# Performance work log

Hardware: AMD Instinct MI355X
Metric: run time of the kernel (lower is better)

## Reference

```python
import jax, jax.numpy as jnp
import numpy as np

BATCH, SEQ, D_MODEL = 8, 4096, 1024
N, K, RHO_MAX, N_POWER_ITER = 16, 4, 0.3, 2
P = N * (N - 1) // 2  # 120 skew params


def _xavier(key, shape, gain):
    fan_out, fan_in = shape
    std = gain * np.sqrt(2.0 / (fan_in + fan_out))
    return jax.random.normal(key, shape, jnp.float32) * std


def setup_inputs() -> dict:
    key = jax.random.key(0)
    k0, k1, k2, k3 = jax.random.split(key, 4)
    u = jax.random.normal(k0, (BATCH, SEQ, D_MODEL), jnp.float32)
    W_proj_w = _xavier(k1, (P, D_MODEL), 0.1)
    W_proj_b = jnp.zeros((P,), jnp.float32)
    B_w = _xavier(k2, (N, D_MODEL), 0.5)
    C_w = _xavier(k3, (D_MODEL, N), 0.5)
    D = jnp.zeros((D_MODEL,), jnp.float32)
    return {"u": u, "W_proj_w": W_proj_w, "W_proj_b": W_proj_b, "B_w": B_w, "C_w": C_w, "D": D}


def _normalize(x, axis):
    # F.normalize: x / max(||x||, eps)
    return x / jnp.maximum(jnp.linalg.norm(x, axis=axis, keepdims=True), 1e-12)


def reference(u, W_proj_w, W_proj_b, B_w, C_w, D):
    Bsz, T, d = u.shape
    n = B_w.shape[0]
    rows, cols = np.triu_indices(n, 1)

    # 1. skew params for all timesteps at once: (B,T,P)
    v = u @ W_proj_w.T + W_proj_b
    A = jnp.zeros((Bsz, T, n, n), u.dtype)
    A = A.at[..., rows, cols].set(v).at[..., cols, rows].set(-v)

    # 2. spectral-norm scaling (power iteration runs with no grad in torch)
    A_sg = jax.lax.stop_gradient(A)
    u_vec = _normalize(jax.random.normal(jax.random.key(1), (Bsz, T, n, 1), u.dtype), axis=2)
    for _ in range(N_POWER_ITER):
        v_vec = _normalize(jnp.swapaxes(A_sg, -1, -2) @ u_vec, axis=2)
        u_vec = _normalize(A_sg @ v_vec, axis=2)
    sigma = jnp.abs((jnp.swapaxes(u_vec, -1, -2) @ (A @ v_vec))[..., 0, 0])  # (B,T)
    scale = RHO_MAX / jnp.maximum(sigma, RHO_MAX)
    A = A * scale[..., None, None]

    # 3. Neumann-Cayley, k=4 radix-2 splitting: W = (I-A)(I+A^2)(I-A)
    I = jnp.eye(n, dtype=u.dtype)
    ImA = I - A
    W = (ImA @ (I + A @ A)) @ ImA  # (B,T,n,n)

    # orthogonality deviation (monitoring, no grad)
    W_sg = jax.lax.stop_gradient(W)
    WtW = jnp.swapaxes(W_sg, -1, -2) @ W_sg
    ortho_dev = jnp.mean(jnp.linalg.norm(WtW - I, axis=(-2, -1)))

    # 4. sequential state recurrence h_t = W_t h_{t-1} + B u_t via scan
    Bx = u @ B_w.T  # (B,T,n)

    def step(h, inp):
        W_t, bx_t = inp  # (B,n,n), (B,n)
        h = jnp.einsum('bij,bj->bi', W_t, h) + bx_t
        return h, h

    h0 = jnp.zeros((Bsz, n), u.dtype)
    _, hs = jax.lax.scan(step, h0, (jnp.swapaxes(W, 0, 1), jnp.swapaxes(Bx, 0, 1)))
    h_all = jnp.swapaxes(hs, 0, 1)  # (B,T,n)

    y = h_all @ C_w.T + u * D
    return y, ortho_dev
```

## Files before the change

kernel.cpp:

```cpp
#include <hip/hip_runtime.h>
#include <hip/hip_bf16.h>
#include <math.h>

#define BATCHN 8
#define SEQN 4096
#define DMODEL 1024
#define MTOT (BATCHN*SEQN)
#define VB_STRIDE 136
#define CHUNKS 64
#define CLEN 64
#define YSIZE ((size_t)MTOT*DMODEL)
#define BN_ROWS 144

typedef __attribute__((ext_vector_type(8))) short short8;
typedef __attribute__((ext_vector_type(4))) float f32x4;

__device__ __forceinline__ unsigned short f2bf(float x){
  __hip_bfloat16 h = __float2bfloat16(x);
  return *(unsigned short*)&h;
}
__device__ __forceinline__ float bf2f(unsigned short b){
  __hip_bfloat16 h; *(unsigned short*)&h = b;
  return __bfloat162float(h);
}

__device__ __forceinline__ unsigned rotl32(unsigned x, int d){ return (x<<d)|(x>>(32-d)); }
__device__ __forceinline__ void tfr(unsigned &x0, unsigned &x1, int r){ x0 += x1; x1 = rotl32(x1,r); x1 ^= x0; }

__device__ __forceinline__ float xla_erfinv(float x){
  float w = -log1pf(-x*x);
  float p;
  if (w < 5.0f){
    w = w - 2.5f;
    p = 2.81022636e-08f;
    p = fmaf(p, w, 3.43273939e-07f);
    p = fmaf(p, w, -3.5233877e-06f);
    p = fmaf(p, w, -4.39150654e-06f);
    p = fmaf(p, w, 0.00021858087f);
    p = fmaf(p, w, -0.00125372503f);
    p = fmaf(p, w, -0.00417768164f);
    p = fmaf(p, w, 0.246640727f);
    p = fmaf(p, w, 1.50140941f);
  } else {
    w = sqrtf(w) - 3.0f;
    p = -0.000200214257f;
    p = fmaf(p, w, 0.000100950558f);
    p = fmaf(p, w, 0.00134934322f);
    p = fmaf(p, w, -0.00367342844f);
    p = fmaf(p, w, 0.00573950773f);
    p = fmaf(p, w, -0.0076224613f);
    p = fmaf(p, w, 0.00943887047f);
    p = fmaf(p, w, 1.00167406f);
    p = fmaf(p, w, 2.83297682f);
  }
  return p * x;
}

__device__ float jax_randn(unsigned I){
  unsigned x0 = 0u, x1 = I;
  const unsigned ks2 = 0x1BD11BDBu;
  x0 += 0u; x1 += 1u;
  tfr(x0,x1,13); tfr(x0,x1,15); tfr(x0,x1,26); tfr(x0,x1,6);
  x0 += 1u; x1 += ks2 + 1u;
  tfr(x0,x1,17); tfr(x0,x1,29); tfr(x0,x1,16); tfr(x0,x1,24);
  x0 += ks2; x1 += 0u + 2u;
  tfr(x0,x1,13); tfr(x0,x1,15); tfr(x0,x1,26); tfr(x0,x1,6);
  x0 += 0u; x1 += 1u + 3u;
  tfr(x0,x1,17); tfr(x0,x1,29); tfr(x0,x1,16); tfr(x0,x1,24);
  x0 += 1u; x1 += ks2 + 4u;
  tfr(x0,x1,13); tfr(x0,x1,15); tfr(x0,x1,26); tfr(x0,x1,6);
  x0 += ks2; x1 += 0u + 5u;
  unsigned bits = x0 ^ x1;
  unsigned fb = (bits >> 9) | 0x3f800000u;
  float f = __uint_as_float(fb) - 1.0f;
  const float lo = -0.99999994f;
  float val = f * 2.0f + lo;
  val = fmaxf(lo, val);
  return 1.4142135381698608f * xla_erfinv(val);
}

__global__ __launch_bounds__(256) void k0_presplit(const float* __restrict__ Wp,
    const float* __restrict__ Bw, unsigned short* __restrict__ Bhi,
    unsigned short* __restrict__ Blo){
  int i = blockIdx.x*256 + threadIdx.x;
  if (i >= BN_ROWS*DMODEL/4) return;
  int n = i >> 8;
  int k = (i & 255) * 4;
  float4 t = make_float4(0.f,0.f,0.f,0.f);
  if (n < 120)      t = *(const float4*)(Wp + (size_t)n*DMODEL + k);
  else if (n < 136) t = *(const float4*)(Bw + (size_t)(n-120)*DMODEL + k);
  unsigned short h[4], l[4];
  float v[4] = {t.x,t.y,t.z,t.w};
  #pragma unroll
  for (int j=0;j<4;j++){
    h[j] = f2bf(v[j]);
    l[j] = f2bf(v[j] - bf2f(h[j]));
  }
  size_t off = (size_t)n*DMODEL + k;
  *(ushort4*)(Bhi + off) = make_ushort4(h[0],h[1],h[2],h[3]);
  *(ushort4*)(Blo + off) = make_ushort4(l[0],l[1],l[2],l[3]);
}

__global__ __launch_bounds__(128) void k1_mfma(const float* __restrict__ u,
    const unsigned short* __restrict__ Bhi, const unsigned short* __restrict__ Blo,
    const float* __restrict__ Wpb, float* __restrict__ vb){
  __shared__ unsigned short As_hi[64*40];
  __shared__ unsigned short As_lo[64*40];
  __shared__ unsigned short Bs_hi[BN_ROWS*40];
  __shared__ unsigned short Bs_lo[BN_ROWS*40];

  const int tid  = threadIdx.x;
  const int wave = tid >> 6;
  const int lane = tid & 63;
  const int quad = lane >> 4;
  const int lrow = lane & 15;
  const int m0   = blockIdx.x * 64;

  float biasv[9];
  #pragma unroll
  for (int t=0;t<9;t++){
    int col = t*16 + lrow;
    biasv[t] = (col < 120) ? Wpb[col] : 0.f;
  }

  f32x4 acc[2][9];
  #pragma unroll
  for (int s=0;s<2;s++)
    #pragma unroll
    for (int t=0;t<9;t++)
      acc[s][t] = (f32x4){0.f,0.f,0.f,0.f};

  const int arow = tid & 63;
  const int ak0  = (tid >> 6) * 16;

  for (int c=0;c<DMODEL/32;c++){
    {
      const float* src = u + (size_t)(m0+arow)*DMODEL + c*32 + ak0;
      float va[16];
      #pragma unroll
      for (int q=0;q<4;q++){
        float4 t4 = *(const float4*)(src + q*4);
        va[q*4+0]=t4.x; va[q*4+1]=t4.y; va[q*4+2]=t4.z; va[q*4+3]=t4.w;
      }
      unsigned short hh[16], ll[16];
      #pragma unroll
      for (int j=0;j<16;j++){
        hh[j] = f2bf(va[j]);
        ll[j] = f2bf(va[j] - bf2f(hh[j]));
      }
      unsigned short* dh = As_hi + arow*40 + ak0;
      unsigned short* dl = As_lo + arow*40 + ak0;
      #pragma unroll
      for (int half=0; half<2; half++){
        short8 ph, pl;
        #pragma unroll
        for (int j=0;j<8;j++){ ph[j] = (short)hh[half*8+j]; pl[j] = (short)ll[half*8+j]; }
        *(short8*)(dh + half*8) = ph;
        *(short8*)(dl + half*8) = pl;
      }
    }
    for (int i = tid; i < BN_ROWS*4; i += 128){
      int n  = i >> 2;
      int kq = (i & 3) * 8;
      size_t goff = (size_t)n*DMODEL + c*32 + kq;
      *(short8*)(Bs_hi + n*40 + kq) = *(const short8*)(Bhi + goff);
      *(short8*)(Bs_lo + n*40 + kq) = *(const short8*)(Blo + goff);
    }
    __syncthreads();

    short8 ahi[2], alo[2];
    #pragma unroll
    for (int s=0;s<2;s++){
      int row = wave*32 + s*16 + lrow;
      ahi[s] = *(const short8*)(As_hi + row*40 + quad*8);
      alo[s] = *(const short8*)(As_lo + row*40 + quad*8);
    }
    #pragma unroll
    for (int t=0;t<9;t++){
      short8 bhi = *(const short8*)(Bs_hi + (t*16+lrow)*40 + quad*8);
      short8 blo = *(const short8*)(Bs_lo + (t*16+lrow)*40 + quad*8);
      #pragma unroll
      for (int s=0;s<2;s++){
        acc[s][t] = __builtin_amdgcn_mfma_f32_16x16x32_bf16(ahi[s], bhi, acc[s][t], 0,0,0);
        acc[s][t] = __builtin_amdgcn_mfma_f32_16x16x32_bf16(ahi[s], blo, acc[s][t], 0,0,0);
        acc[s][t] = __builtin_amdgcn_mfma_f32_16x16x32_bf16(alo[s], bhi, acc[s][t], 0,0,0);
      }
    }
    __syncthreads();
  }

  #pragma unroll
  for (int s=0;s<2;s++){
    #pragma unroll
    for (int t=0;t<9;t++){
      int col = t*16 + lrow;
      if (col < VB_STRIDE){
        #pragma unroll
        for (int i=0;i<4;i++){
          int row = m0 + wave*32 + s*16 + quad*4 + i;
          vb[(size_t)row*VB_STRIDE + col] = acc[s][t][i] + biasv[t];
        }
      }
    }
  }
}

__global__ __launch_bounds__(128) void k2_build_w(const float* __restrict__ vb,
    float* __restrict__ Wg, float* __restrict__ ortho){
  __shared__ float Af[8*324];
  __shared__ float Sf[8*324];
  __shared__ float gsum[8];
  const int tid = threadIdx.x;
  const int grp = tid >> 4;
  const int r   = tid & 15;
  const int m   = blockIdx.x*8 + grp;
  float* A = Af + grp*324;
  float* S = Sf + grp*324;
  const float* vrow = vb + (size_t)m*VB_STRIDE;

  float a_s[16];
  #pragma unroll
  for (int c=0;c<16;c++){
    float val = 0.f;
    if (c > r)      val =  vrow[r*15 - (r*(r-1))/2 + (c-r-1)];
    else if (c < r) val = -vrow[c*15 - (c*(c-1))/2 + (r-c-1)];
    a_s[c] = val;
  }

  float uv = jax_randn((unsigned)m*16u + (unsigned)r);
  float nn = uv*uv;
  #pragma unroll
  for (int s=1;s<16;s<<=1) nn += __shfl_xor(nn, s, 16);
  uv = uv / fmaxf(sqrtf(nn), 1e-12f);

  float t2 = 0.f;
  #pragma unroll
  for (int it=0; it<2; ++it){
    float t1 = 0.f;
    #pragma unroll
    for (int k=0;k<16;k++) t1 += a_s[k]*__shfl(uv, k, 16);
    t1 = -t1;
    nn = t1*t1;
    #pragma unroll
    for (int s=1;s<16;s<<=1) nn += __shfl_xor(nn, s, 16);
    float vvec = t1 / fmaxf(sqrtf(nn), 1e-12f);
    t2 = 0.f;
    #pragma unroll
    for (int k=0;k<16;k++) t2 += a_s[k]*__shfl(vvec, k, 16);
    nn = t2*t2;
    #pragma unroll
    for (int s=1;s<16;s<<=1) nn += __shfl_xor(nn, s, 16);
    uv = t2 / fmaxf(sqrtf(nn), 1e-12f);
  }
  float sig = uv * t2;
  #pragma unroll
  for (int s=1;s<16;s<<=1) sig += __shfl_xor(sig, s, 16);
  sig = fabsf(sig);
  const float scale = 0.3f / fmaxf(sig, 0.3f);
  #pragma unroll
  for (int k=0;k<16;k++) a_s[k] *= scale;

  #pragma unroll
  for (int q=0;q<4;q++)
    *(float4*)(A + r*20 + q*4) = make_float4(a_s[q*4],a_s[q*4+1],a_s[q*4+2],a_s[q*4+3]);
  __syncthreads();

  float s_s[16];
  #pragma unroll
  for (int j=0;j<16;j++) s_s[j] = 0.f;
  #pragma unroll
  for (int k=0;k<16;k++){
    #pragma unroll
    for (int q=0;q<4;q++){
      float4 ak = *(const float4*)(A + k*20 + q*4);
      s_s[q*4+0] = fmaf(a_s[k], ak.x, s_s[q*4+0]);
      s_s[q*4+1] = fmaf(a_s[k], ak.y, s_s[q*4+1]);
      s_s[q*4+2] = fmaf(a_s[k], ak.z, s_s[q*4+2]);
      s_s[q*4+3] = fmaf(a_s[k], ak.w, s_s[q*4+3]);
    }
  }
  #pragma unroll
  for (int q=0;q<4;q++)
    *(float4*)(S + r*20 + q*4) = make_float4(s_s[q*4],s_s[q*4+1],s_s[q*4+2],s_s[q*4+3]);
  __syncthreads();

  float as_s[16], ss_s[16];
  #pragma unroll
  for (int j=0;j<16;j++){ as_s[j]=0.f; ss_s[j]=0.f; }
  #pragma unroll
  for (int k=0;k<16;k++){
    #pragma unroll
    for (int q=0;q<4;q++){
      float4 sk = *(const float4*)(S + k*20 + q*4);
      as_s[q*4+0] = fmaf(a_s[k], sk.x, as_s[q*4+0]);
      as_s[q*4+1] = fmaf(a_s[k], sk.y, as_s[q*4+1]);
      as_s[q*4+2] = fmaf(a_s[k], sk.z, as_s[q*4+2]);
      as_s[q*4+3] = fmaf(a_s[k], sk.w, as_s[q*4+3]);
      ss_s[q*4+0] = fmaf(s_s[k], sk.x, ss_s[q*4+0]);
      ss_s[q*4+1] = fmaf(s_s[k], sk.y, ss_s[q*4+1]);
      ss_s[q*4+2] = fmaf(s_s[k], sk.z, ss_s[q*4+2]);
      ss_s[q*4+3] = fmaf(s_s[k], sk.w, ss_s[q*4+3]);
    }
  }
  float w_s[16];
  #pragma unroll
  for (int j=0;j<16;j++){
    float wv = -2.f*a_s[j] + 2.f*s_s[j] - 2.f*as_s[j] + ss_s[j];
    if (j == r) wv += 1.f;
    w_s[j] = wv;
  }
  float4* wout = (float4*)(Wg + (size_t)m*256 + r*16);
  #pragma unroll
  for (int q=0;q<4;q++)
    wout[q] = make_float4(w_s[q*4],w_s[q*4+1],w_s[q*4+2],w_s[q*4+3]);

  __syncthreads();
  #pragma unroll
  for (int q=0;q<4;q++)
    *(float4*)(A + r*20 + q*4) = make_float4(w_s[q*4],w_s[q*4+1],w_s[q*4+2],w_s[q*4+3]);
  __syncthreads();
  float wt_s[16];
  #pragma unroll
  for (int j=0;j<16;j++) wt_s[j] = 0.f;
  #pragma unroll
  for (int k=0;k<16;k++){
    float ck = A[k*20 + r];
    #pragma unroll
    for (int q=0;q<4;q++){
      float4 wk = *(const float4*)(A + k*20 + q*4);
      wt_s[q*4+0] = fmaf(ck, wk.x, wt_s[q*4+0]);
      wt_s[q*4+1] = fmaf(ck, wk.y, wt_s[q*4+1]);
      wt_s[q*4+2] = fmaf(ck, wk.z, wt_s[q*4+2]);
      wt_s[q*4+3] = fmaf(ck, wk.w, wt_s[q*4+3]);
    }
  }
  float dev = 0.f;
  #pragma unroll
  for (int j=0;j<16;j++){
    float v = wt_s[j] - ((j==r)?1.f:0.f);
    dev += v*v;
  }
  #pragma unroll
  for (int s=1;s<16;s<<=1) dev += __shfl_xor(dev, s, 16);
  if (r==0) gsum[grp] = sqrtf(dev);
  __syncthreads();
  if (tid==0){
    float t=0.f;
    #pragma unroll
    for (int i=0;i<8;i++) t += gsum[i];
    atomicAdd(ortho, t);
  }
}

__global__ __launch_bounds__(64) void k3a_chunk_reduce(const float* __restrict__ Wg,
    const float* __restrict__ vb, double* __restrict__ Msum){
  const int chunk = blockIdx.x;
  const int b = chunk >> 6, c = chunk & 63;
  const int lane = threadIdx.x, r = lane & 15, g = lane >> 4;
  __shared__ double Mb[2][16*20];
  __shared__ double sb[16];
  #pragma unroll
  for (int cc=0;cc<4;cc++) Mb[0][r*20 + 4*g + cc] = (r == 4*g+cc) ? 1.0 : 0.0;
  if (lane < 16) sb[lane] = 0.0;
  __syncthreads();
  const size_t mbase = (size_t)b*SEQN + (size_t)c*CLEN;
  float4 wq = *(const float4*)(Wg + mbase*256 + r*16 + 4*g);
  float bx = vb[mbase*VB_STRIDE + 120 + r];
  int p = 0;
  for (int t=0;t<CLEN;++t){
    float4 wn = make_float4(0.f,0.f,0.f,0.f); float bxn = 0.f;
    if (t+1 < CLEN){
      wn  = *(const float4*)(Wg + (mbase+t+1)*256 + r*16 + 4*g);
      bxn = vb[(mbase+t+1)*VB_STRIDE + 120 + r];
    }
    const double* M = Mb[p];
    double a0=0.0,a1=0.0,a2=0.0,a3=0.0, sacc=0.0;
    #pragma unroll
    for (int kg=0;kg<4;kg++){
      float wk0 = __shfl(wq.x, r + 16*kg);
      float wk1 = __shfl(wq.y, r + 16*kg);
      float wk2 = __shfl(wq.z, r + 16*kg);
      float wk3 = __shfl(wq.w, r + 16*kg);
      float wkv[4] = {wk0,wk1,wk2,wk3};
      #pragma unroll
      for (int e=0;e<4;e++){
        int k = 4*kg + e;
        double w = (double)wkv[e];
        const double* mrow = M + k*20 + 4*g;
        a0 = fma(w, mrow[0], a0);
        a1 = fma(w, mrow[1], a1);
        a2 = fma(w, mrow[2], a2);
        a3 = fma(w, mrow[3], a3);
        sacc = fma(w, sb[k], sacc);
      }
    }
    __syncthreads();
    double* Mn = Mb[1-p];
    Mn[r*20+4*g+0]=a0; Mn[r*20+4*g+1]=a1; Mn[r*20+4*g+2]=a2; Mn[r*20+4*g+3]=a3;
    if (g==0) sb[r] = sacc + (double)bx;
    __syncthreads();
    p ^= 1;
    wq = wn; bx = bxn;
  }
  double* out = Msum + (size_t)chunk*272;
  #pragma unroll
  for (int cc=0;cc<4;cc++) out[r*16+4*g+cc] = Mb[p][r*20+4*g+cc];
  if (lane<16) out[256+lane] = sb[lane];
}

__global__ __launch_bounds__(64) void k3b_prefix(const double* __restrict__ Msum,
    double* __restrict__ hstart){
  const int b = blockIdx.x;
  const int lane = threadIdx.x, r = lane & 15, g = lane >> 4;
  __shared__ double q[16];
  if (lane < 16) q[lane] = 0.0;
  __syncthreads();
  const double* base = Msum + (size_t)b*CHUNKS*272;
  double2 m01 = *(const double2*)(base + r*16 + 4*g);
  double2 m23 = *(const double2*)(base + r*16 + 4*g + 2);
  double sv = base[256 + r];
  for (int c=0;c<CHUNKS;++c){
    double2 n01, n23; double svn = 0.0;
    n01.x=n01.y=n23.x=n23.y=0.0;
    if (c+1 < CHUNKS){
      const double* bn = base + (size_t)(c+1)*272;
      n01 = *(const double2*)(bn + r*16 + 4*g);
      n23 = *(const double2*)(bn + r*16 + 4*g + 2);
      svn = bn[256 + r];
    }
    if (lane < 16) hstart[((size_t)b*CHUNKS + c)*16 + lane] = q[lane];
    double part = m01.x*q[4*g+0] + m01.y*q[4*g+1] + m23.x*q[4*g+2] + m23.y*q[4*g+3];
    part += __shfl_xor(part, 16);
    part += __shfl_xor(part, 32);
    __syncthreads();
    if (g==0) q[r] = part + sv;
    __syncthreads();
    m01 = n01; m23 = n23; sv = svn;
  }
}

__global__ __launch_bounds__(64) void k3c_apply(const float* __restrict__ Wg,
    const float* __restrict__ vb, const double* __restrict__ hstart,
    float* __restrict__ hout){
  const int chunk = blockIdx.x;
  const int b = chunk >> 6, c = chunk & 63;
  const int lane = threadIdx.x, r = lane & 15, g = lane >> 4;
  __shared__ double h[16];
  if (lane < 16) h[lane] = hstart[(size_t)chunk*16 + lane];
  __syncthreads();
  const size_t mbase = (size_t)b*SEQN + (size_t)c*CLEN;
  float4 wq = *(const float4*)(Wg + mbase*256 + r*16 + 4*g);
  float bx = vb[mbase*VB_STRIDE + 120 + r];
  for (int t=0;t<CLEN;++t){
    float4 wn = make_float4(0.f,0.f,0.f,0.f); float bxn = 0.f;
    if (t+1 < CLEN){
      wn  = *(const float4*)(Wg + (mbase+t+1)*256 + r*16 + 4*g);
      bxn = vb[(mbase+t+1)*VB_STRIDE + 120 + r];
    }
    double part = (double)wq.x*h[4*g+0] + (double)wq.y*h[4*g+1]
                + (double)wq.z*h[4*g+2] + (double)wq.w*h[4*g+3];
    part += __shfl_xor(part, 16);
    part += __shfl_xor(part, 32);
    __syncthreads();
    if (g==0){
      double nh = part + (double)bx;
      h[r] = nh;
      hout[(mbase+t)*16 + r] = (float)nh;
    }
    __syncthreads();
    wq = wn; bx = bxn;
  }
}

__device__ __forceinline__ float dot4f(float4 a, float4 b){
  return a.x*b.x + a.y*b.y + a.z*b.z + a.w*b.w;
}

__global__ __launch_bounds__(256) void k4_out(const float* __restrict__ hbuf,
    const float* __restrict__ u, const float* __restrict__ Cw,
    const float* __restrict__ D, const float* __restrict__ ortho,
    float* __restrict__ y, int write_ortho){
  __shared__ float hl[256];
  const int m0 = blockIdx.x * 16;
  hl[threadIdx.x] = hbuf[(size_t)m0*16 + threadIdx.x];
  __syncthreads();
  const int col = threadIdx.x * 4;
  float4 cm[4][4];
  #pragma unroll
  for (int cc=0;cc<4;cc++)
    #pragma unroll
    for (int jj=0;jj<4;jj++)
      cm[cc][jj] = *(const float4*)(Cw + (size_t)(col+cc)*16 + jj*4);
  float4 d4 = *(const float4*)(D + col);
  #pragma unroll
  for (int row=0;row<16;row++){
    const float4* hr = (const float4*)(hl + row*16);
    float4 h0=hr[0], h1=hr[1], h2=hr[2], h3=hr[3];
    float4 o;
    o.x = dot4f(cm[0][0],h0)+dot4f(cm[0][1],h1)+dot4f(cm[0][2],h2)+dot4f(cm[0][3],h3);
    o.y = dot4f(cm[1][0],h0)+dot4f(cm[1][1],h1)+dot4f(cm[1][2],h2)+dot4f(cm[1][3],h3);
    o.z = dot4f(cm[2][0],h0)+dot4f(cm[2][1],h1)+dot4f(cm[2][2],h2)+dot4f(cm[2][3],h3);
    o.w = dot4f(cm[3][0],h0)+dot4f(cm[3][1],h1)+dot4f(cm[3][2],h2)+dot4f(cm[3][3],h3);
    size_t off = (size_t)(m0+row)*DMODEL + col;
    float4 u4 = *(const float4*)(u + off);
    o.x += u4.x*d4.x; o.y += u4.y*d4.y; o.z += u4.z*d4.z; o.w += u4.w*d4.w;
    *(float4*)(y + off) = o;
  }
  if (write_ortho && blockIdx.x==0 && threadIdx.x==0)
    y[YSIZE] = ortho[0] * (1.0f/32768.0f);
}

extern "C" void kernel_launch(void* const* d_in, const int* in_sizes, int n_in,
                              void* d_out, int out_size, void* d_ws, size_t ws_size,
                              hipStream_t stream){
  const float* u   = (const float*)d_in[0];
  const float* Wp  = (const float*)d_in[1];
  const float* Wpb = (const float*)d_in[2];
  const float* Bw  = (const float*)d_in[3];
  const float* Cw  = (const float*)d_in[4];
  const float* D   = (const float*)d_in[5];
  float* y = (float*)d_out;

  float* f      = (float*)d_ws;
  float* vb     = f;
  float* Wg     = vb  + (size_t)MTOT*VB_STRIDE;
  float* hbuf   = Wg  + (size_t)MTOT*256;
  double* Msum  = (double*)(hbuf + (size_t)MTOT*16);
  double* hstart= Msum + (size_t)BATCHN*CHUNKS*272;
  unsigned short* Bhi = (unsigned short*)(hstart + (size_t)BATCHN*CHUNKS*16);
  unsigned short* Blo = Bhi + (size_t)BN_ROWS*DMODEL;
  float* ortho  = (float*)(Blo + (size_t)BN_ROWS*DMODEL);

  int write_ortho = ((size_t)out_size > YSIZE) ? 1 : 0;

  hipMemsetAsync(ortho, 0, sizeof(float), stream);
  hipLaunchKernelGGL(k0_presplit,     dim3((BN_ROWS*DMODEL/4+255)/256), dim3(256), 0, stream, Wp, Bw, Bhi, Blo);
  hipLaunchKernelGGL(k1_mfma,         dim3(MTOT/64), dim3(128), 0, stream, u, Bhi, Blo, Wpb, vb);
  hipLaunchKernelGGL(k2_build_w,      dim3(MTOT/8), dim3(128), 0, stream, vb, Wg, ortho);
  hipLaunchKernelGGL(k3a_chunk_reduce,dim3(BATCHN*CHUNKS), dim3(64), 0, stream, Wg, vb, Msum);
  hipLaunchKernelGGL(k3b_prefix,      dim3(BATCHN), dim3(64), 0, stream, Msum, hstart);
  hipLaunchKernelGGL(k3c_apply,       dim3(BATCHN*CHUNKS), dim3(64), 0, stream, Wg, vb, hstart, hbuf);
  hipLaunchKernelGGL(k4_out,          dim3(MTOT/16), dim3(256), 0, stream, hbuf, u, Cw, D, ortho, y, write_ortho);
}
```

Measured before the change: 503.0 us.

## Double-buffer k1 GEMM with 8-wave blocks and halve scan chunk length

Rewrites the projection GEMM kernel to use 512-thread blocks split 4x2 across M and N tiles. The B tile is double-buffered in LDS with register prefetch of the next K-slice, and A is loaded directly into registers and split hi/lo per wave, so the A shared-memory stage goes away. This is meant to overlap global loads with MFMA work and raise occupancy. Separately, the recurrence scan uses 128 chunks of length 32 instead of 64x64, giving more parallel blocks in the chunk-reduce and apply kernels at the cost of a longer sequential prefix.

```diff
diff --git a/kernel.cpp b/kernel.cpp
--- a/kernel.cpp
+++ b/kernel.cpp
@@ -7,8 +7,8 @@
 #define DMODEL 1024
 #define MTOT (BATCHN*SEQN)
 #define VB_STRIDE 136
-#define CHUNKS 64
-#define CLEN 64
+#define CHUNKS 128
+#define CLEN 32
 #define YSIZE ((size_t)MTOT*DMODEL)
 #define BN_ROWS 144
 
@@ -101,104 +101,116 @@
   *(ushort4*)(Blo + off) = make_ushort4(l[0],l[1],l[2],l[3]);
 }
 
-__global__ __launch_bounds__(128) void k1_mfma(const float* __restrict__ u,
+#define K1_THREADS 512
+#define K1_BUNITS (2*BN_ROWS*4)
+
+__global__ __launch_bounds__(512, 4) void k1_mfma(const float* __restrict__ u,
     const unsigned short* __restrict__ Bhi, const unsigned short* __restrict__ Blo,
     const float* __restrict__ Wpb, float* __restrict__ vb){
-  __shared__ unsigned short As_hi[64*40];
-  __shared__ unsigned short As_lo[64*40];
-  __shared__ unsigned short Bs_hi[BN_ROWS*40];
-  __shared__ unsigned short Bs_lo[BN_ROWS*40];
+  __shared__ unsigned short Bs[2][2*BN_ROWS*40];
 
   const int tid  = threadIdx.x;
-  const int wave = tid >> 6;
+  const int wid  = tid >> 6;
   const int lane = tid & 63;
   const int quad = lane >> 4;
   const int lrow = lane & 15;
+  const int wm   = wid & 3;
+  const int wn   = wid >> 2;
+  const int t0   = wn ? 5 : 0;
+  const int nt   = wn ? 4 : 5;
   const int m0   = blockIdx.x * 64;
 
-  float biasv[9];
-  #pragma unroll
-  for (int t=0;t<9;t++){
-    int col = t*16 + lrow;
-    biasv[t] = (col < 120) ? Wpb[col] : 0.f;
-  }
-
-  f32x4 acc[2][9];
-  #pragma unroll
-  for (int s=0;s<2;s++)
-    #pragma unroll
-    for (int t=0;t<9;t++)
-      acc[s][t] = (f32x4){0.f,0.f,0.f,0.f};
-
-  const int arow = tid & 63;
-  const int ak0  = (tid >> 6) * 16;
+  const float* aptr = u + (size_t)(m0 + wm*16 + lrow)*DMODEL + quad*8;
+
+  float biasv[5];
+  #pragma unroll
+  for (int t=0;t<5;t++){
+    int col = (t0+t)*16 + lrow;
+    biasv[t] = (t < nt && col < 120) ? Wpb[col] : 0.f;
+  }
+
+  f32x4 acc[5];
+  #pragma unroll
+  for (int t=0;t<5;t++) acc[t] = (f32x4){0.f,0.f,0.f,0.f};
+
+  for (int i=tid; i<K1_BUNITS; i+=K1_THREADS){
+    int half = (i >= BN_ROWS*4) ? 1 : 0;
+    int j = i - half*BN_ROWS*4;
+    int n = j >> 2, kq = (j & 3)*8;
+    const unsigned short* src = (half ? Blo : Bhi) + (size_t)n*DMODEL + kq;
+    *(short8*)(&Bs[0][half*BN_ROWS*40 + n*40 + kq]) = *(const short8*)src;
+  }
+  float4 af0 = *(const float4*)(aptr);
+  float4 af1 = *(const float4*)(aptr + 4);
+  short8 ahi, alo;
+  {
+    float va[8] = {af0.x,af0.y,af0.z,af0.w,af1.x,af1.y,af1.z,af1.w};
+    #pragma unroll
+    for (int j=0;j<8;j++){
+      unsigned short h = f2bf(va[j]);
+      ahi[j] = (short)h;
+      alo[j] = (short)f2bf(va[j] - bf2f(h));
+    }
+  }
+  __syncthreads();
 
   for (int c=0;c<DMODEL/32;c++){
-    {
-      const float* src = u + (size_t)(m0+arow)*DMODEL + c*32 + ak0;
-      float va[16];
+    const int cur = c & 1;
+    short8 breg[3]; int nb = 0;
+    float4 an0, an1;
+    const bool more = (c+1 < DMODEL/32);
+    if (more){
+      const float* ap = aptr + (c+1)*32;
+      an0 = *(const float4*)(ap);
+      an1 = *(const float4*)(ap + 4);
+      for (int i=tid; i<K1_BUNITS; i+=K1_THREADS){
+        int half = (i >= BN_ROWS*4) ? 1 : 0;
+        int j = i - half*BN_ROWS*4;
+        int n = j >> 2, kq = (j & 3)*8;
+        breg[nb++] = *(const short8*)((half ? Blo : Bhi) + (size_t)n*DMODEL + (size_t)(c+1)*32 + kq);
+      }
+    }
+    const unsigned short* bh = &Bs[cur][0];
+    const unsigned short* bl = &Bs[cur][BN_ROWS*40];
+    #pragma unroll
+    for (int t=0;t<5;t++){
+      if (t < nt){
+        const int n = (t0+t)*16 + lrow;
+        short8 bhi8 = *(const short8*)(bh + n*40 + quad*8);
+        short8 blo8 = *(const short8*)(bl + n*40 + quad*8);
+        acc[t] = __builtin_amdgcn_mfma_f32_16x16x32_bf16(ahi, bhi8, acc[t], 0,0,0);
+        acc[t] = __builtin_amdgcn_mfma_f32_16x16x32_bf16(ahi, blo8, acc[t], 0,0,0);
+        acc[t] = __builtin_amdgcn_mfma_f32_16x16x32_bf16(alo, bhi8, acc[t], 0,0,0);
+      }
+    }
+    if (more){
+      nb = 0;
+      for (int i=tid; i<K1_BUNITS; i+=K1_THREADS){
+        int half = (i >= BN_ROWS*4) ? 1 : 0;
+        int j = i - half*BN_ROWS*4;
+        int n = j >> 2, kq = (j & 3)*8;
+        *(short8*)(&Bs[1-cur][half*BN_ROWS*40 + n*40 + kq]) = breg[nb++];
+      }
+      float va[8] = {an0.x,an0.y,an0.z,an0.w,an1.x,an1.y,an1.z,an1.w};
       #pragma unroll
-      for (int q=0;q<4;q++){
-        float4 t4 = *(const float4*)(src + q*4);
-        va[q*4+0]=t4.x; va[q*4+1]=t4.y; va[q*4+2]=t4.z; va[q*4+3]=t4.w;
+      for (int j=0;j<8;j++){
+        unsigned short h = f2bf(va[j]);
+        ahi[j] = (short)h;
+        alo[j] = (short)f2bf(va[j] - bf2f(h));
       }
-      unsigned short hh[16], ll[16];
-      #pragma unroll
-      for (int j=0;j<16;j++){
-        hh[j] = f2bf(va[j]);
-        ll[j] = f2bf(va[j] - bf2f(hh[j]));
-      }
-      unsigned short* dh = As_hi + arow*40 + ak0;
-      unsigned short* dl = As_lo + arow*40 + ak0;
-      #pragma unroll
-      for (int half=0; half<2; half++){
-        short8 ph, pl;
-        #pragma unroll
-        for (int j=0;j<8;j++){ ph[j] = (short)hh[half*8+j]; pl[j] = (short)ll[half*8+j]; }
-        *(short8*)(dh + half*8) = ph;
-        *(short8*)(dl + half*8) = pl;
-      }
-    }
-    for (int i = tid; i < BN_ROWS*4; i += 128){
-      int n  = i >> 2;
-      int kq = (i & 3) * 8;
-      size_t goff = (size_t)n*DMODEL + c*32 + kq;
-      *(short8*)(Bs_hi + n*40 + kq) = *(const short8*)(Bhi + goff);
-      *(short8*)(Bs_lo + n*40 + kq) = *(const short8*)(Blo + goff);
-    }
-    __syncthreads();
-
-    short8 ahi[2], alo[2];
-    #pragma unroll
-    for (int s=0;s<2;s++){
-      int row = wave*32 + s*16 + lrow;
-      ahi[s] = *(const short8*)(As_hi + row*40 + quad*8);
-      alo[s] = *(const short8*)(As_lo + row*40 + quad*8);
-    }
-    #pragma unroll
-    for (int t=0;t<9;t++){
-      short8 bhi = *(const short8*)(Bs_hi + (t*16+lrow)*40 + quad*8);
-      short8 blo = *(const short8*)(Bs_lo + (t*16+lrow)*40 + quad*8);
-      #pragma unroll
-      for (int s=0;s<2;s++){
-        acc[s][t] = __builtin_amdgcn_mfma_f32_16x16x32_bf16(ahi[s], bhi, acc[s][t], 0,0,0);
-        acc[s][t] = __builtin_amdgcn_mfma_f32_16x16x32_bf16(ahi[s], blo, acc[s][t], 0,0,0);
-        acc[s][t] = __builtin_amdgcn_mfma_f32_16x16x32_bf16(alo[s], bhi, acc[s][t], 0,0,0);
-      }
-    }
-    __syncthreads();
-  }
-
-  #pragma unroll
-  for (int s=0;s<2;s++){
-    #pragma unroll
-    for (int t=0;t<9;t++){
-      int col = t*16 + lrow;
+    }
+    __syncthreads();
+  }
+
+  #pragma unroll
+  for (int t=0;t<5;t++){
+    if (t < nt){
+      int col = (t0+t)*16 + lrow;
       if (col < VB_STRIDE){
         #pragma unroll
         for (int i=0;i<4;i++){
-          int row = m0 + wave*32 + s*16 + quad*4 + i;
-          vb[(size_t)row*VB_STRIDE + col] = acc[s][t][i] + biasv[t];
+          int row = m0 + wm*16 + quad*4 + i;
+          vb[(size_t)row*VB_STRIDE + col] = acc[t][i] + biasv[t];
         }
       }
     }
@@ -355,7 +367,7 @@
 __global__ __launch_bounds__(64) void k3a_chunk_reduce(const float* __restrict__ Wg,
     const float* __restrict__ vb, double* __restrict__ Msum){
   const int chunk = blockIdx.x;
-  const int b = chunk >> 6, c = chunk & 63;
+  const int b = chunk / CHUNKS, c = chunk - b*CHUNKS;
   const int lane = threadIdx.x, r = lane & 15, g = lane >> 4;
   __shared__ double Mb[2][16*20];
   __shared__ double sb[16];
@@ -443,7 +455,7 @@
     const float* __restrict__ vb, const double* __restrict__ hstart,
     float* __restrict__ hout){
   const int chunk = blockIdx.x;
-  const int b = chunk >> 6, c = chunk & 63;
+  const int b = chunk / CHUNKS, c = chunk - b*CHUNKS;
   const int lane = threadIdx.x, r = lane & 15, g = lane >> 4;
   __shared__ double h[16];
   if (lane < 16) h[lane] = hstart[(size_t)chunk*16 + lane];
@@ -535,7 +547,7 @@
 
   hipMemsetAsync(ortho, 0, sizeof(float), stream);
   hipLaunchKernelGGL(k0_presplit,     dim3((BN_ROWS*DMODEL/4+255)/256), dim3(256), 0, stream, Wp, Bw, Bhi, Blo);
-  hipLaunchKernelGGL(k1_mfma,         dim3(MTOT/64), dim3(128), 0, stream, u, Bhi, Blo, Wpb, vb);
+  hipLaunchKernelGGL(k1_mfma,         dim3(MTOT/64), dim3(K1_THREADS), 0, stream, u, Bhi, Blo, Wpb, vb);
   hipLaunchKernelGGL(k2_build_w,      dim3(MTOT/8), dim3(128), 0, stream, vb, Wg, ortho);
   hipLaunchKernelGGL(k3a_chunk_reduce,dim3(BATCHN*CHUNKS), dim3(64), 0, stream, Wg, vb, Msum);
   hipLaunchKernelGGL(k3b_prefix,      dim3(BATCHN), dim3(64), 0, stream, Msum, hstart);
```

Result: slower. 985.9 us (+96.0%).
